# Performance work log

Hardware: AMD Instinct MI355X
Metric: run time of the kernel (lower is better)

Reference implementation:

```python
import jax, jax.numpy as jnp
import numpy as np

N_LAYERS, D_MODEL, D_INNER, D_STATE, DT_RANK, D_CONV, VOCAB = 4, 768, 1536, 16, 48, 4, 32000
B, L = 2, 512
EPS = 1e-5


def rmsnorm(x, w):
    var = jnp.mean(jnp.square(x), axis=-1, keepdims=True)
    return x * jax.lax.rsqrt(var + EPS) * w


def mamba_mixer(x, in_w, cw, cb, xp_w, dtp_w, dtp_b, A_log, D_sk, out_w):
    # x: [B, L, D]
    proj = x @ in_w.T                                   # [B, L, 2*d_inner]
    h, gate = jnp.split(proj, 2, axis=-1)
    hc = jnp.transpose(h, (0, 2, 1))                    # [B, d_inner, L]
    hc = jax.lax.conv_general_dilated(
        hc, cw[:, None, :], (1,), [(D_CONV - 1, 0)],
        dimension_numbers=('NCH', 'OIH', 'NCH'),
        feature_group_count=D_INNER) + cb[None, :, None]  # causal depthwise conv
    h = jax.nn.silu(jnp.transpose(hc, (0, 2, 1)))       # [B, L, d_inner]
    ssm = h @ xp_w.T                                    # [B, L, dt_rank + 2*d_state]
    dt, Bm, Cm = jnp.split(ssm, [DT_RANK, DT_RANK + D_STATE], axis=-1)
    dt = jax.nn.softplus(dt @ dtp_w.T + dtp_b)          # [B, L, d_inner]
    A = -jnp.exp(A_log)                                 # [d_inner, d_state], always negative
    dA = jnp.exp(dt[..., None] * A)                     # [B, L, d_inner, d_state]
    dBu = (dt * h)[..., None] * Bm[:, :, None, :]       # [B, L, d_inner, d_state]

    def step(state, inp):
        dA_t, dBu_t, C_t = inp
        state = dA_t * state + dBu_t                    # [B, d_inner, d_state]
        return state, jnp.einsum('bds,bs->bd', state, C_t)

    xs = (jnp.moveaxis(dA, 1, 0), jnp.moveaxis(dBu, 1, 0), jnp.moveaxis(Cm, 1, 0))
    init = jnp.zeros((x.shape[0], D_INNER, D_STATE), dtype=x.dtype)
    _, ys = jax.lax.scan(step, init, xs)                # ys: [L, B, d_inner]
    y = jnp.moveaxis(ys, 0, 1) + D_sk * h
    y = y * jax.nn.silu(gate)
    return y @ out_w.T                                  # [B, L, D]


def setup_inputs() -> dict:
    key = jax.random.key(0)
    ks = jax.random.split(key, 8)
    inp = {
        'input_ids': jax.random.randint(ks[0], (B, L), 0, VOCAB, dtype=jnp.int32),
        'embed': jax.random.normal(ks[1], (VOCAB, D_MODEL), jnp.float32) * 0.02,
        'norm_f_w': jnp.ones((D_MODEL,), jnp.float32),
        'in_proj_w': jax.random.normal(ks[2], (N_LAYERS, 2 * D_INNER, D_MODEL), jnp.float32) * (D_MODEL ** -0.5),
        'conv_w': jax.random.normal(ks[3], (N_LAYERS, D_INNER, D_CONV), jnp.float32) * 0.3,
        'conv_b': jnp.zeros((N_LAYERS, D_INNER), jnp.float32),
        'x_proj_w': jax.random.normal(ks[4], (N_LAYERS, DT_RANK + 2 * D_STATE, D_INNER), jnp.float32) * (D_INNER ** -0.5),
        'dt_proj_w': jax.random.normal(ks[5], (N_LAYERS, D_INNER, DT_RANK), jnp.float32) * (DT_RANK ** -0.5),
        'dt_proj_b': jax.random.normal(ks[6], (N_LAYERS, D_INNER), jnp.float32) * 0.1,
        'A_log': jnp.broadcast_to(jnp.log(jnp.arange(1, D_STATE + 1, dtype=jnp.float32)), (N_LAYERS, D_INNER, D_STATE)).copy(),
        'D_skip': jnp.ones((N_LAYERS, D_INNER), jnp.float32),
        'out_proj_w': jax.random.normal(ks[7], (N_LAYERS, D_MODEL, D_INNER), jnp.float32) * (D_INNER ** -0.5),
        'norm_w': jnp.ones((N_LAYERS, D_MODEL), jnp.float32),
    }
    return inp


def reference(input_ids, embed, norm_f_w, in_proj_w, conv_w, conv_b,
              x_proj_w, dt_proj_w, dt_proj_b, A_log, D_skip, out_proj_w, norm_w):
    h = embed[input_ids]                                # [B, L, D]
    for i in range(N_LAYERS):
        h = h + mamba_mixer(rmsnorm(h, norm_w[i]), in_proj_w[i], conv_w[i], conv_b[i],
                            x_proj_w[i], dt_proj_w[i], dt_proj_b[i],
                            A_log[i], D_skip[i], out_proj_w[i])
    h = rmsnorm(h, norm_f_w)
    return h @ embed.T                                  # tied lm head logits [B, L, VOCAB]
```

## Files before the change

### kernel.cpp

```cpp
#include <hip/hip_runtime.h>
#include <hip/hip_bf16.h>
#include <math.h>

#define NL 4
#define DM 768
#define DI 1536
#define DS 16
#define DTR 48
#define DCONV 4
#define VOCAB_ 32000
#define BB 2
#define LL 512
#define ROWS (BB*LL)
#define SSMW (DTR + 2*DS)
#define NC 32
#define CL (LL/NC)
#define NDB (DI/16)
#define XP_KS 16
#define XP_KC (DI/XP_KS)

typedef __bf16 bf16x8 __attribute__((ext_vector_type(8)));
typedef float f32x4 __attribute__((ext_vector_type(4)));

__device__ __forceinline__ unsigned short f2bf(float f) {
    unsigned u = __float_as_uint(f);
    u = u + 0x7fffu + ((u >> 16) & 1u);
    return (unsigned short)(u >> 16);
}
__device__ __forceinline__ float bf2f(unsigned short b) {
    return __uint_as_float((unsigned)b << 16);
}

__global__ __launch_bounds__(256) void split_kernel(
    const float* __restrict__ x,
    unsigned short* __restrict__ hi, unsigned short* __restrict__ lo, int n4)
{
    int i = blockIdx.x * 256 + threadIdx.x;
    if (i >= n4) return;
    const float4 v = ((const float4*)x)[i];
    float vv[4] = {v.x, v.y, v.z, v.w};
    unsigned short hh[4], ll[4];
    #pragma unroll
    for (int j = 0; j < 4; j++) {
        hh[j] = f2bf(vv[j]);
        ll[j] = f2bf(vv[j] - bf2f(hh[j]));
    }
    ((ushort4*)hi)[i] = make_ushort4(hh[0], hh[1], hh[2], hh[3]);
    ((ushort4*)lo)[i] = make_ushort4(ll[0], ll[1], ll[2], ll[3]);
}

__device__ __forceinline__ void gld16(void* l, const void* g) {
    __builtin_amdgcn_global_load_lds(
        (const __attribute__((address_space(1))) void*)g,
        (__attribute__((address_space(3))) void*)l, 16, 0, 0);
}

template<int EPI>
__global__ __launch_bounds__(256) void gemm_mfma(
    const unsigned short* __restrict__ Ahi, const unsigned short* __restrict__ Alo, int lda,
    const unsigned short* __restrict__ Bhi, const unsigned short* __restrict__ Blo, int ldb,
    float* __restrict__ C, int ldc, int K,
    const float* __restrict__ resid)
{
    __shared__ __align__(16) unsigned short sAh[128*32];
    __shared__ __align__(16) unsigned short sAl[128*32];
    __shared__ __align__(16) unsigned short sBh[128*32];
    __shared__ __align__(16) unsigned short sBl[128*32];

    const int tid  = threadIdx.x;
    const int lane = tid & 63;
    const int m0 = blockIdx.x * 128;
    const int n0 = blockIdx.y * 128;
    const int w  = tid >> 6;
    const int wr = (w >> 1) * 64;
    const int wc = (w & 1) * 64;

    f32x4 acc[4][4];
    #pragma unroll
    for (int i = 0; i < 4; i++)
        #pragma unroll
        for (int j = 0; j < 4; j++)
            acc[i][j] = (f32x4){0.f, 0.f, 0.f, 0.f};

    const int srow = tid >> 2;
    const int ps   = tid & 3;
    const int lsl  = ps ^ ((srow >> 1) & 3);

    int offA[4], offB[4];
    #pragma unroll
    for (int i = 0; i < 4; i++) {
        int ra = wr + i*16 + (lane & 15);
        int pa = (lane >> 4) ^ ((ra >> 1) & 3);
        offA[i] = ra*32 + pa*8;
        int rb = wc + i*16 + (lane & 15);
        int pb = (lane >> 4) ^ ((rb >> 1) & 3);
        offB[i] = rb*32 + pb*8;
    }

    for (int k0 = 0; k0 < K; k0 += 32) {
        const size_t a1 = (size_t)(m0 + srow)      * lda + k0 + lsl*8;
        const size_t a2 = (size_t)(m0 + 64 + srow) * lda + k0 + lsl*8;
        const size_t b1 = (size_t)(n0 + srow)      * ldb + k0 + lsl*8;
        const size_t b2 = (size_t)(n0 + 64 + srow) * ldb + k0 + lsl*8;
        gld16(&sAh[(size_t)tid*8],       Ahi + a1);
        gld16(&sAh[(size_t)(256+tid)*8], Ahi + a2);
        gld16(&sAl[(size_t)tid*8],       Alo + a1);
        gld16(&sAl[(size_t)(256+tid)*8], Alo + a2);
        gld16(&sBh[(size_t)tid*8],       Bhi + b1);
        gld16(&sBh[(size_t)(256+tid)*8], Bhi + b2);
        gld16(&sBl[(size_t)tid*8],       Blo + b1);
        gld16(&sBl[(size_t)(256+tid)*8], Blo + b2);
        __syncthreads();

        bf16x8 ah[4], al[4], bh[4], bl[4];
        #pragma unroll
        for (int i = 0; i < 4; i++) {
            ah[i] = *(const bf16x8*)&sAh[offA[i]];
            al[i] = *(const bf16x8*)&sAl[offA[i]];
            bh[i] = *(const bf16x8*)&sBh[offB[i]];
            bl[i] = *(const bf16x8*)&sBl[offB[i]];
        }
        #pragma unroll
        for (int i = 0; i < 4; i++)
            #pragma unroll
            for (int j = 0; j < 4; j++) {
                acc[i][j] = __builtin_amdgcn_mfma_f32_16x16x32_bf16(ah[i], bh[j], acc[i][j], 0, 0, 0);
                acc[i][j] = __builtin_amdgcn_mfma_f32_16x16x32_bf16(ah[i], bl[j], acc[i][j], 0, 0, 0);
                acc[i][j] = __builtin_amdgcn_mfma_f32_16x16x32_bf16(al[i], bh[j], acc[i][j], 0, 0, 0);
            }
        __syncthreads();
    }

    #pragma unroll
    for (int i = 0; i < 4; i++) {
        int rbase = m0 + wr + i*16 + (lane >> 4)*4;
        #pragma unroll
        for (int j = 0; j < 4; j++) {
            int col = n0 + wc + j*16 + (lane & 15);
            #pragma unroll
            for (int r = 0; r < 4; r++) {
                float v = acc[i][j][r];
                if (EPI == 2) v += resid[(size_t)(rbase + r)*ldc + col];
                C[(size_t)(rbase + r)*ldc + col] = v;
            }
        }
    }
}

__global__ __launch_bounds__(256) void gather_kernel(
    const int* __restrict__ ids, const float* __restrict__ embed,
    float* __restrict__ h, int n)
{
    int idx = blockIdx.x * 256 + threadIdx.x;
    if (idx >= n) return;
    int d = idx % DM;
    int tok = idx / DM;
    h[idx] = embed[(size_t)ids[tok] * DM + d];
}

__global__ __launch_bounds__(256) void rmsnorm_kernel(
    const float* __restrict__ x, const float* __restrict__ w,
    float* __restrict__ out, int D)
{
    int row = blockIdx.x;
    const float* xr = x + (size_t)row * D;
    float ss = 0.f;
    for (int i = threadIdx.x; i < D; i += 256) { float v = xr[i]; ss += v * v; }
    for (int o = 32; o >= 1; o >>= 1) ss += __shfl_xor(ss, o, 64);
    __shared__ float sbuf[4];
    int wid = threadIdx.x >> 6;
    if ((threadIdx.x & 63) == 0) sbuf[wid] = ss;
    __syncthreads();
    if (threadIdx.x == 0) {
        float t = sbuf[0] + sbuf[1] + sbuf[2] + sbuf[3];
        sbuf[0] = 1.0f / sqrtf(t / (float)D + 1e-5f);
    }
    __syncthreads();
    float scale = sbuf[0];
    for (int i = threadIdx.x; i < D; i += 256)
        out[(size_t)row * D + i] = xr[i] * scale * w[i];
}

template<int EPI>
__global__ __launch_bounds__(256) void gemm_tn(
    const float* __restrict__ A, int lda,
    const float* __restrict__ W, int ldw,
    float* __restrict__ C, int ldc,
    int M, int N, int K,
    const float* __restrict__ bias,
    const float* __restrict__ resid)
{
    const int tid = threadIdx.x;
    const int tx = tid & 15;
    const int ty = tid >> 4;
    const int m0 = blockIdx.x * 64;
    const int n0 = blockIdx.y * 64;

    __shared__ float As[16][65];
    __shared__ float Ws[16][65];

    float acc[4][4];
    #pragma unroll
    for (int i = 0; i < 4; i++)
        #pragma unroll
        for (int j = 0; j < 4; j++) acc[i][j] = 0.f;

    const int lrow = tid >> 2;
    const int lk   = (tid & 3) * 4;

    for (int k0 = 0; k0 < K; k0 += 16) {
        {
            int m = m0 + lrow;
            int n = n0 + lrow;
            #pragma unroll
            for (int j = 0; j < 4; j++) {
                int k = k0 + lk + j;
                As[lk + j][lrow] = (m < M && k < K) ? A[(size_t)m * lda + k] : 0.f;
                Ws[lk + j][lrow] = (n < N && k < K) ? W[(size_t)n * ldw + k] : 0.f;
            }
        }
        __syncthreads();
        #pragma unroll
        for (int k = 0; k < 16; k++) {
            float a[4], wv[4];
            #pragma unroll
            for (int i = 0; i < 4; i++) a[i] = As[k][ty * 4 + i];
            #pragma unroll
            for (int j = 0; j < 4; j++) wv[j] = Ws[k][tx * 4 + j];
            #pragma unroll
            for (int i = 0; i < 4; i++)
                #pragma unroll
                for (int j = 0; j < 4; j++)
                    acc[i][j] += a[i] * wv[j];
        }
        __syncthreads();
    }

    #pragma unroll
    for (int i = 0; i < 4; i++) {
        int m = m0 + ty * 4 + i;
        if (m >= M) continue;
        #pragma unroll
        for (int j = 0; j < 4; j++) {
            int n = n0 + tx * 4 + j;
            if (n >= N) continue;
            float v = acc[i][j];
            if (EPI == 1) {
                v += bias[n];
                v = fmaxf(v, 0.f) + log1pf(expf(-fabsf(v)));
            }
            if (EPI == 2) v += resid[(size_t)m * ldc + n];
            C[(size_t)m * ldc + n] = v;
        }
    }
}

__global__ __launch_bounds__(256) void xproj_partial_kernel(
    const float* __restrict__ A,
    const float* __restrict__ W,
    float* __restrict__ part)
{
    __shared__ float sA[32*97];
    __shared__ float sW[80*97];
    const int m0 = blockIdx.x * 32;
    const int k0 = blockIdx.y * XP_KC;

    for (int idx = threadIdx.x; idx < 32*XP_KC; idx += 256) {
        int r = idx / XP_KC, k = idx % XP_KC;
        sA[r*97 + k] = A[(size_t)(m0 + r)*DI + k0 + k];
    }
    for (int idx = threadIdx.x; idx < 80*XP_KC; idx += 256) {
        int r = idx / XP_KC, k = idx % XP_KC;
        sW[r*97 + k] = W[(size_t)r*DI + k0 + k];
    }
    __syncthreads();

    const int tr = (threadIdx.x >> 4) * 2;
    const int tc = (threadIdx.x & 15) * 5;
    float acc[2][5];
    #pragma unroll
    for (int i = 0; i < 2; i++)
        #pragma unroll
        for (int j = 0; j < 5; j++) acc[i][j] = 0.f;

    #pragma unroll 4
    for (int k = 0; k < XP_KC; ++k) {
        float a0 = sA[tr*97 + k];
        float a1 = sA[(tr+1)*97 + k];
        float w0 = sW[(tc+0)*97 + k];
        float w1 = sW[(tc+1)*97 + k];
        float w2 = sW[(tc+2)*97 + k];
        float w3 = sW[(tc+3)*97 + k];
        float w4 = sW[(tc+4)*97 + k];
        acc[0][0] += a0*w0; acc[0][1] += a0*w1; acc[0][2] += a0*w2;
        acc[0][3] += a0*w3; acc[0][4] += a0*w4;
        acc[1][0] += a1*w0; acc[1][1] += a1*w1; acc[1][2] += a1*w2;
        acc[1][3] += a1*w3; acc[1][4] += a1*w4;
    }

    float* pp = part + ((size_t)blockIdx.y * ROWS + m0) * SSMW;
    #pragma unroll
    for (int i = 0; i < 2; i++)
        #pragma unroll
        for (int j = 0; j < 5; j++)
            pp[(size_t)(tr + i)*SSMW + tc + j] = acc[i][j];
}

__global__ __launch_bounds__(256) void xproj_reduce_kernel(
    const float* __restrict__ part, float* __restrict__ ssmout)
{
    int i = blockIdx.x * 256 + threadIdx.x;
    if (i >= ROWS * SSMW) return;
    float s = 0.f;
    #pragma unroll
    for (int ks = 0; ks < XP_KS; ++ks)
        s += part[(size_t)ks * ROWS * SSMW + i];
    ssmout[i] = s;
}

__global__ __launch_bounds__(256) void conv_silu_kernel(
    const float* __restrict__ proj,
    const float* __restrict__ cw, const float* __restrict__ cb,
    float* __restrict__ hconv)
{
    int idx = blockIdx.x * 256 + threadIdx.x;
    if (idx >= ROWS * DI) return;
    int d = idx % DI;
    int bt = idx / DI;
    int t = bt % LL;
    float sum = cb[d];
    #pragma unroll
    for (int j = 0; j < DCONV; j++) {
        int tt = t - (DCONV - 1) + j;
        if (tt >= 0)
            sum += cw[d * DCONV + j] * proj[(size_t)(bt - (DCONV - 1) + j) * (2 * DI) + d];
    }
    float sig = 1.f / (1.f + expf(-sum));
    hconv[idx] = sum * sig;
}

__global__ __launch_bounds__(256) void scan_local_kernel(
    const float* __restrict__ dt, const float* __restrict__ hconv,
    const float* __restrict__ ssm, const float* __restrict__ A_log,
    float* __restrict__ ylocal, float* __restrict__ E, float* __restrict__ P)
{
    const int tid = threadIdx.x;
    const int s  = tid & 15;
    const int dg = tid >> 4;
    int blk = blockIdx.x;
    const int dblk = blk % NDB; blk /= NDB;
    const int c = blk % NC;
    const int b = blk / NC;
    const int d = dblk * 16 + dg;

    const float Ads = -expf(A_log[(size_t)d * DS + s]);
    float state = 0.f, Ssum = 0.f;
    const int t0 = c * CL;
    const float* dtp = dt     + ((size_t)b*LL + t0)*DI + d;
    const float* hp  = hconv  + ((size_t)b*LL + t0)*DI + d;
    const float* sp  = ssm    + ((size_t)b*LL + t0)*SSMW;
    float*       yp  = ylocal + ((size_t)b*LL + t0)*DI + d;

    for (int t = 0; t < CL; ++t) {
        float dtv = dtp[(size_t)t * DI];
        float hv  = hp[(size_t)t * DI];
        float Bv  = sp[(size_t)t * SSMW + DTR + s];
        float Cv  = sp[(size_t)t * SSMW + DTR + DS + s];
        float dA  = expf(dtv * Ads);
        state = dA * state + dtv * hv * Bv;
        Ssum += dtv;
        float contrib = state * Cv;
        contrib += __shfl_xor(contrib, 1, 16);
        contrib += __shfl_xor(contrib, 2, 16);
        contrib += __shfl_xor(contrib, 4, 16);
        contrib += __shfl_xor(contrib, 8, 16);
        if (s == 0) yp[(size_t)t * DI] = contrib;
    }
    const size_t si = (((size_t)b*NC + c)*DI + d)*DS + s;
    E[si] = state;
    P[si] = expf(Ads * Ssum);
}

__global__ __launch_bounds__(256) void scan_carry_kernel(
    const float* __restrict__ E, const float* __restrict__ P,
    float* __restrict__ carry)
{
    int g = blockIdx.x * 256 + threadIdx.x;
    if (g >= BB * DI * DS) return;
    int b   = g / (DI * DS);
    int dsi = g % (DI * DS);
    float cv = 0.f;
    for (int c = 0; c < NC; ++c) {
        size_t idx = ((size_t)b*NC + c)*(DI*DS) + dsi;
        carry[idx] = cv;
        cv = P[idx] * cv + E[idx];
    }
}

__global__ __launch_bounds__(256) void scan_fix_kernel(
    const float* __restrict__ dt, const float* __restrict__ hconv,
    const float* __restrict__ ssm, const float* __restrict__ proj,
    const float* __restrict__ A_log, const float* __restrict__ D_skip,
    const float* __restrict__ carry, float* __restrict__ y)
{
    const int tid = threadIdx.x;
    const int s  = tid & 15;
    const int dg = tid >> 4;
    int blk = blockIdx.x;
    const int dblk = blk % NDB; blk /= NDB;
    const int c = blk % NC;
    const int b = blk / NC;
    const int d = dblk * 16 + dg;

    const float Ads = -expf(A_log[(size_t)d * DS + s]);
    const float Dd  = D_skip[d];
    const float cv  = carry[(((size_t)b*NC + c)*DI + d)*DS + s];
    float S = 0.f;
    const int t0 = c * CL;
    const float* dtp = dt    + ((size_t)b*LL + t0)*DI + d;
    const float* hp  = hconv + ((size_t)b*LL + t0)*DI + d;
    const float* sp  = ssm   + ((size_t)b*LL + t0)*SSMW;
    const float* gp  = proj  + ((size_t)b*LL + t0)*(2*DI) + DI + d;
    float*       yp  = y     + ((size_t)b*LL + t0)*DI + d;

    for (int t = 0; t < CL; ++t) {
        float dtv = dtp[(size_t)t * DI];
        S += dtv;
        float Cv = sp[(size_t)t * SSMW + DTR + DS + s];
        float contrib = expf(Ads * S) * cv * Cv;
        contrib += __shfl_xor(contrib, 1, 16);
        contrib += __shfl_xor(contrib, 2, 16);
        contrib += __shfl_xor(contrib, 4, 16);
        contrib += __shfl_xor(contrib, 8, 16);
        if (s == 0) {
            float hv  = hp[(size_t)t * DI];
            float ylo = yp[(size_t)t * DI];
            float gv  = gp[(size_t)t * (2*DI)];
            float sig = 1.f / (1.f + expf(-gv));
            yp[(size_t)t * DI] = (ylo + contrib + Dd * hv) * (gv * sig);
        }
    }
}

extern "C" void kernel_launch(void* const* d_in, const int* in_sizes, int n_in,
                              void* d_out, int out_size, void* d_ws, size_t ws_size,
                              hipStream_t stream)
{
    const int*   ids        = (const int*)  d_in[0];
    const float* embed      = (const float*)d_in[1];
    const float* norm_f_w   = (const float*)d_in[2];
    const float* in_proj_w  = (const float*)d_in[3];
    const float* conv_w     = (const float*)d_in[4];
    const float* conv_b     = (const float*)d_in[5];
    const float* x_proj_w   = (const float*)d_in[6];
    const float* dt_proj_w  = (const float*)d_in[7];
    const float* dt_proj_b  = (const float*)d_in[8];
    const float* A_log      = (const float*)d_in[9];
    const float* D_skip     = (const float*)d_in[10];
    const float* out_proj_w = (const float*)d_in[11];
    const float* norm_w     = (const float*)d_in[12];
    float* out = (float*)d_out;

    float* ws    = (float*)d_ws;
    float* h     = ws;
    float* xn    = h     + ROWS * DM;
    float* proj  = xn    + ROWS * DM;
    float* hconv = proj  + ROWS * 2 * DI;
    float* ssm   = hconv + ROWS * DI;
    float* dtb   = ssm   + ROWS * SSMW;
    float* yb    = dtb   + ROWS * DI;
    float* Ebuf  = yb    + ROWS * DI;
    float* Pbuf  = Ebuf  + (size_t)BB*NC*DI*DS;
    float* cbuf  = Pbuf  + (size_t)BB*NC*DI*DS;
    float* xpart = cbuf  + (size_t)BB*NC*DI*DS;
    const size_t F32_FLOATS = (size_t)ROWS * (DM + DM + 2*DI + DI + SSMW + DI + DI)
                            + 3 * (size_t)BB*NC*DI*DS
                            + (size_t)XP_KS*ROWS*SSMW;

    const size_t IPW_E = (size_t)NL * 2 * DI * DM;
    const size_t OPW_E = (size_t)NL * DM * DI;
    const size_t ACT_E = (size_t)ROWS * DI;
    const size_t EMB_E = (size_t)VOCAB_ * DM;
    unsigned short* u0   = (unsigned short*)(ws + F32_FLOATS);
    unsigned short* ipwh = u0;
    unsigned short* ipwl = ipwh + IPW_E;
    unsigned short* opwh = ipwl + IPW_E;
    unsigned short* opwl = opwh + OPW_E;
    unsigned short* acth = opwl + OPW_E;
    unsigned short* actl = acth + ACT_E;
    unsigned short* embh = actl + ACT_E;
    unsigned short* embl = embh + EMB_E;
    const size_t NEED_PROJ = F32_FLOATS*4 + 2*2*(IPW_E + OPW_E + ACT_E);
    const size_t NEED_HEAD = NEED_PROJ + 2*2*EMB_E;
    const bool mfma_proj = ws_size >= NEED_PROJ;
    const bool mfma_head = ws_size >= NEED_HEAD;

    gather_kernel<<<(ROWS * DM + 255) / 256, 256, 0, stream>>>(ids, embed, h, ROWS * DM);

    if (mfma_proj) {
        split_kernel<<<(int)(IPW_E/4 + 255)/256, 256, 0, stream>>>(in_proj_w,  ipwh, ipwl, (int)(IPW_E/4));
        split_kernel<<<(int)(OPW_E/4 + 255)/256, 256, 0, stream>>>(out_proj_w, opwh, opwl, (int)(OPW_E/4));
    }
    if (mfma_head) {
        split_kernel<<<(int)(EMB_E/4 + 255)/256, 256, 0, stream>>>(embed, embh, embl, (int)(EMB_E/4));
    }

    for (int i = 0; i < NL; ++i) {
        const float* ipw = in_proj_w  + (size_t)i * 2 * DI * DM;
        const float* cw  = conv_w     + (size_t)i * DI * DCONV;
        const float* cb  = conv_b     + (size_t)i * DI;
        const float* xpw = x_proj_w   + (size_t)i * SSMW * DI;
        const float* dpw = dt_proj_w  + (size_t)i * DI * DTR;
        const float* dpb = dt_proj_b  + (size_t)i * DI;
        const float* al  = A_log      + (size_t)i * DI * DS;
        const float* dsk = D_skip     + (size_t)i * DI;
        const float* opw = out_proj_w + (size_t)i * DM * DI;
        const float* nw  = norm_w     + (size_t)i * DM;

        rmsnorm_kernel<<<ROWS, 256, 0, stream>>>(h, nw, xn, DM);

        if (mfma_proj) {
            split_kernel<<<(ROWS*DM/4 + 255)/256, 256, 0, stream>>>(xn, acth, actl, ROWS*DM/4);
            gemm_mfma<0><<<dim3(ROWS/128, (2*DI)/128), 256, 0, stream>>>(
                acth, actl, DM, ipwh + (size_t)i*2*DI*DM, ipwl + (size_t)i*2*DI*DM, DM,
                proj, 2*DI, DM, nullptr);
        } else {
            gemm_tn<0><<<dim3(ROWS/64, (2*DI)/64), 256, 0, stream>>>(
                xn, DM, ipw, DM, proj, 2*DI, ROWS, 2*DI, DM, nullptr, nullptr);
        }

        conv_silu_kernel<<<(ROWS * DI + 255) / 256, 256, 0, stream>>>(proj, cw, cb, hconv);

        xproj_partial_kernel<<<dim3(ROWS/32, XP_KS), 256, 0, stream>>>(hconv, xpw, xpart);
        xproj_reduce_kernel<<<(ROWS*SSMW + 255)/256, 256, 0, stream>>>(xpart, ssm);

        gemm_tn<1><<<dim3(ROWS / 64, DI / 64), 256, 0, stream>>>(
            ssm, SSMW, dpw, DTR, dtb, DI, ROWS, DI, DTR, dpb, nullptr);

        scan_local_kernel<<<BB*NC*NDB, 256, 0, stream>>>(dtb, hconv, ssm, al, yb, Ebuf, Pbuf);
        scan_carry_kernel<<<(BB*DI*DS + 255)/256, 256, 0, stream>>>(Ebuf, Pbuf, cbuf);
        scan_fix_kernel<<<BB*NC*NDB, 256, 0, stream>>>(dtb, hconv, ssm, proj, al, dsk, cbuf, yb);

        if (mfma_proj) {
            split_kernel<<<(ROWS*DI/4 + 255)/256, 256, 0, stream>>>(yb, acth, actl, ROWS*DI/4);
            gemm_mfma<2><<<dim3(ROWS/128, DM/128), 256, 0, stream>>>(
                acth, actl, DI, opwh + (size_t)i*DM*DI, opwl + (size_t)i*DM*DI, DI,
                h, DM, DI, h);
        } else {
            gemm_tn<2><<<dim3(ROWS/64, DM/64), 256, 0, stream>>>(
                yb, DI, opw, DI, h, DM, ROWS, DM, DI, nullptr, h);
        }
    }

    rmsnorm_kernel<<<ROWS, 256, 0, stream>>>(h, norm_f_w, xn, DM);
    if (mfma_head) {
        split_kernel<<<(ROWS*DM/4 + 255)/256, 256, 0, stream>>>(xn, acth, actl, ROWS*DM/4);
        gemm_mfma<0><<<dim3(ROWS/128, VOCAB_/128), 256, 0, stream>>>(
            acth, actl, DM, embh, embl, DM, out, VOCAB_, DM, nullptr);
    } else {
        gemm_tn<0><<<dim3(ROWS/64, VOCAB_/64), 256, 0, stream>>>(
            xn, DM, embed, DM, out, VOCAB_, ROWS, VOCAB_, DM, nullptr, nullptr);
    }
}
```

Baseline: 1.434 ms.

## Fuse rmsnorm/scan epilogues with bf16 split, split-K out_proj, remap GEMM blocks

Folds the hi/lo bf16 split into the rmsnorm kernel and into the scan_fix epilogue, removing the separate split launches and their fp32 round trips. The out_proj MFMA GEMM now runs split-K over 4 slices into a partial buffer, followed by a reduce kernel that adds the residual, to raise the block count from 48. GEMM launches use a 1D grid with a block-index remap meant to improve L2 locality. The cost is an extra partial-sum buffer and reduce pass, plus a different summation order.

```diff
diff --git a/kernel.cpp b/kernel.cpp
--- a/kernel.cpp
+++ b/kernel.cpp
@@ -18,6 +18,8 @@
 #define NDB (DI/16)
 #define XP_KS 16
 #define XP_KC (DI/XP_KS)
+#define OP_KS 4
+#define OP_KC (DI/OP_KS)
 
 typedef __bf16 bf16x8 __attribute__((ext_vector_type(8)));
 typedef float f32x4 __attribute__((ext_vector_type(4)));
@@ -60,7 +62,7 @@
     const unsigned short* __restrict__ Ahi, const unsigned short* __restrict__ Alo, int lda,
     const unsigned short* __restrict__ Bhi, const unsigned short* __restrict__ Blo, int ldb,
     float* __restrict__ C, int ldc, int K,
-    const float* __restrict__ resid)
+    const float* __restrict__ resid, int gx, size_t zstride)
 {
     __shared__ __align__(16) unsigned short sAh[128*32];
     __shared__ __align__(16) unsigned short sAl[128*32];
@@ -69,8 +71,13 @@
 
     const int tid  = threadIdx.x;
     const int lane = tid & 63;
-    const int m0 = blockIdx.x * 128;
-    const int n0 = blockIdx.y * 128;
+    const int nb = gridDim.x;
+    const int v  = (blockIdx.x & 7) * (nb >> 3) + (blockIdx.x >> 3);
+    const int m0 = (v % gx) * 128;
+    const int n0 = (v / gx) * 128;
+    const int kb = (int)blockIdx.y * K;
+    C += (size_t)blockIdx.y * zstride;
+
     const int w  = tid >> 6;
     const int wr = (w >> 1) * 64;
     const int wc = (w & 1) * 64;
@@ -97,7 +104,7 @@
         offB[i] = rb*32 + pb*8;
     }
 
-    for (int k0 = 0; k0 < K; k0 += 32) {
+    for (int k0 = kb; k0 < kb + K; k0 += 32) {
         const size_t a1 = (size_t)(m0 + srow)      * lda + k0 + lsl*8;
         const size_t a2 = (size_t)(m0 + 64 + srow) * lda + k0 + lsl*8;
         const size_t b1 = (size_t)(n0 + srow)      * ldb + k0 + lsl*8;
@@ -139,12 +146,24 @@
             int col = n0 + wc + j*16 + (lane & 15);
             #pragma unroll
             for (int r = 0; r < 4; r++) {
-                float v = acc[i][j][r];
-                if (EPI == 2) v += resid[(size_t)(rbase + r)*ldc + col];
-                C[(size_t)(rbase + r)*ldc + col] = v;
+                float vv = acc[i][j][r];
+                if (EPI == 2) vv += resid[(size_t)(rbase + r)*ldc + col];
+                C[(size_t)(rbase + r)*ldc + col] = vv;
             }
         }
     }
+}
+
+__global__ __launch_bounds__(256) void opart_reduce_kernel(
+    const float* __restrict__ part, float* __restrict__ h, int n)
+{
+    int i = blockIdx.x * 256 + threadIdx.x;
+    if (i >= n) return;
+    float s = h[i];
+    #pragma unroll
+    for (int z = 0; z < OP_KS; ++z)
+        s += part[(size_t)z * n + i];
+    h[i] = s;
 }
 
 __global__ __launch_bounds__(256) void gather_kernel(
@@ -179,6 +198,33 @@
     float scale = sbuf[0];
     for (int i = threadIdx.x; i < D; i += 256)
         out[(size_t)row * D + i] = xr[i] * scale * w[i];
+}
+
+__global__ __launch_bounds__(256) void rmsnorm_split_kernel(
+    const float* __restrict__ x, const float* __restrict__ w,
+    unsigned short* __restrict__ hi, unsigned short* __restrict__ lo, int D)
+{
+    int row = blockIdx.x;
+    const float* xr = x + (size_t)row * D;
+    float ss = 0.f;
+    for (int i = threadIdx.x; i < D; i += 256) { float v = xr[i]; ss += v * v; }
+    for (int o = 32; o >= 1; o >>= 1) ss += __shfl_xor(ss, o, 64);
+    __shared__ float sbuf[4];
+    int wid = threadIdx.x >> 6;
+    if ((threadIdx.x & 63) == 0) sbuf[wid] = ss;
+    __syncthreads();
+    if (threadIdx.x == 0) {
+        float t = sbuf[0] + sbuf[1] + sbuf[2] + sbuf[3];
+        sbuf[0] = 1.0f / sqrtf(t / (float)D + 1e-5f);
+    }
+    __syncthreads();
+    float scale = sbuf[0];
+    for (int i = threadIdx.x; i < D; i += 256) {
+        float v = xr[i] * scale * w[i];
+        unsigned short hh = f2bf(v);
+        hi[(size_t)row * D + i] = hh;
+        lo[(size_t)row * D + i] = f2bf(v - bf2f(hh));
+    }
 }
 
 template<int EPI>
@@ -397,11 +443,13 @@
     }
 }
 
+template<int PLANES>
 __global__ __launch_bounds__(256) void scan_fix_kernel(
     const float* __restrict__ dt, const float* __restrict__ hconv,
     const float* __restrict__ ssm, const float* __restrict__ proj,
     const float* __restrict__ A_log, const float* __restrict__ D_skip,
-    const float* __restrict__ carry, float* __restrict__ y)
+    const float* __restrict__ carry, float* __restrict__ y,
+    unsigned short* __restrict__ yhi, unsigned short* __restrict__ ylo)
 {
     const int tid = threadIdx.x;
     const int s  = tid & 15;
@@ -421,7 +469,7 @@
     const float* hp  = hconv + ((size_t)b*LL + t0)*DI + d;
     const float* sp  = ssm   + ((size_t)b*LL + t0)*SSMW;
     const float* gp  = proj  + ((size_t)b*LL + t0)*(2*DI) + DI + d;
-    float*       yp  = y     + ((size_t)b*LL + t0)*DI + d;
+    const size_t yoff = ((size_t)b*LL + t0)*DI + d;
 
     for (int t = 0; t < CL; ++t) {
         float dtv = dtp[(size_t)t * DI];
@@ -434,10 +482,17 @@
         contrib += __shfl_xor(contrib, 8, 16);
         if (s == 0) {
             float hv  = hp[(size_t)t * DI];
-            float ylo = yp[(size_t)t * DI];
+            float ylv = y[yoff + (size_t)t * DI];
             float gv  = gp[(size_t)t * (2*DI)];
             float sig = 1.f / (1.f + expf(-gv));
-            yp[(size_t)t * DI] = (ylo + contrib + Dd * hv) * (gv * sig);
+            float yv  = (ylv + contrib + Dd * hv) * (gv * sig);
+            if (PLANES) {
+                unsigned short hh = f2bf(yv);
+                yhi[yoff + (size_t)t * DI] = hh;
+                ylo[yoff + (size_t)t * DI] = f2bf(yv - bf2f(hh));
+            } else {
+                y[yoff + (size_t)t * DI] = yv;
+            }
         }
     }
 }
@@ -473,9 +528,11 @@
     float* Pbuf  = Ebuf  + (size_t)BB*NC*DI*DS;
     float* cbuf  = Pbuf  + (size_t)BB*NC*DI*DS;
     float* xpart = cbuf  + (size_t)BB*NC*DI*DS;
+    float* opart = xpart + (size_t)XP_KS*ROWS*SSMW;
     const size_t F32_FLOATS = (size_t)ROWS * (DM + DM + 2*DI + DI + SSMW + DI + DI)
                             + 3 * (size_t)BB*NC*DI*DS
-                            + (size_t)XP_KS*ROWS*SSMW;
+                            + (size_t)XP_KS*ROWS*SSMW
+                            + (size_t)OP_KS*ROWS*DM;
 
     const size_t IPW_E = (size_t)NL * 2 * DI * DM;
     const size_t OPW_E = (size_t)NL * DM * DI;
@@ -517,14 +574,13 @@
         const float* opw = out_proj_w + (size_t)i * DM * DI;
         const float* nw  = norm_w     + (size_t)i * DM;
 
-        rmsnorm_kernel<<<ROWS, 256, 0, stream>>>(h, nw, xn, DM);
-
         if (mfma_proj) {
-            split_kernel<<<(ROWS*DM/4 + 255)/256, 256, 0, stream>>>(xn, acth, actl, ROWS*DM/4);
-            gemm_mfma<0><<<dim3(ROWS/128, (2*DI)/128), 256, 0, stream>>>(
+            rmsnorm_split_kernel<<<ROWS, 256, 0, stream>>>(h, nw, acth, actl, DM);
+            gemm_mfma<0><<<dim3(8*24, 1), 256, 0, stream>>>(
                 acth, actl, DM, ipwh + (size_t)i*2*DI*DM, ipwl + (size_t)i*2*DI*DM, DM,
-                proj, 2*DI, DM, nullptr);
+                proj, 2*DI, DM, nullptr, 8, 0);
         } else {
+            rmsnorm_kernel<<<ROWS, 256, 0, stream>>>(h, nw, xn, DM);
             gemm_tn<0><<<dim3(ROWS/64, (2*DI)/64), 256, 0, stream>>>(
                 xn, DM, ipw, DM, proj, 2*DI, ROWS, 2*DI, DM, nullptr, nullptr);
         }
@@ -539,25 +595,28 @@
 
         scan_local_kernel<<<BB*NC*NDB, 256, 0, stream>>>(dtb, hconv, ssm, al, yb, Ebuf, Pbuf);
         scan_carry_kernel<<<(BB*DI*DS + 255)/256, 256, 0, stream>>>(Ebuf, Pbuf, cbuf);
-        scan_fix_kernel<<<BB*NC*NDB, 256, 0, stream>>>(dtb, hconv, ssm, proj, al, dsk, cbuf, yb);
 
         if (mfma_proj) {
-            split_kernel<<<(ROWS*DI/4 + 255)/256, 256, 0, stream>>>(yb, acth, actl, ROWS*DI/4);
-            gemm_mfma<2><<<dim3(ROWS/128, DM/128), 256, 0, stream>>>(
+            scan_fix_kernel<1><<<BB*NC*NDB, 256, 0, stream>>>(
+                dtb, hconv, ssm, proj, al, dsk, cbuf, yb, acth, actl);
+            gemm_mfma<0><<<dim3(8*6, OP_KS), 256, 0, stream>>>(
                 acth, actl, DI, opwh + (size_t)i*DM*DI, opwl + (size_t)i*DM*DI, DI,
-                h, DM, DI, h);
+                opart, DM, OP_KC, nullptr, 8, (size_t)ROWS*DM);
+            opart_reduce_kernel<<<(ROWS*DM + 255)/256, 256, 0, stream>>>(opart, h, ROWS*DM);
         } else {
+            scan_fix_kernel<0><<<BB*NC*NDB, 256, 0, stream>>>(
+                dtb, hconv, ssm, proj, al, dsk, cbuf, yb, nullptr, nullptr);
             gemm_tn<2><<<dim3(ROWS/64, DM/64), 256, 0, stream>>>(
                 yb, DI, opw, DI, h, DM, ROWS, DM, DI, nullptr, h);
         }
     }
 
-    rmsnorm_kernel<<<ROWS, 256, 0, stream>>>(h, norm_f_w, xn, DM);
     if (mfma_head) {
-        split_kernel<<<(ROWS*DM/4 + 255)/256, 256, 0, stream>>>(xn, acth, actl, ROWS*DM/4);
-        gemm_mfma<0><<<dim3(ROWS/128, VOCAB_/128), 256, 0, stream>>>(
-            acth, actl, DM, embh, embl, DM, out, VOCAB_, DM, nullptr);
+        rmsnorm_split_kernel<<<ROWS, 256, 0, stream>>>(h, norm_f_w, acth, actl, DM);
+        gemm_mfma<0><<<dim3(8*250, 1), 256, 0, stream>>>(
+            acth, actl, DM, embh, embl, DM, out, VOCAB_, DM, nullptr, 8, 0);
     } else {
+        rmsnorm_kernel<<<ROWS, 256, 0, stream>>>(h, norm_f_w, xn, DM);
         gemm_tn<0><<<dim3(ROWS/64, VOCAB_/64), 256, 0, stream>>>(
             xn, DM, embed, DM, out, VOCAB_, ROWS, VOCAB_, DM, nullptr, nullptr);
     }
```

New measurement: 1.238 ms. 1.16x faster.
